# Performance work log

Measured on AMD Instinct MI355X. Metric: run time of the kernel, lower is better.

Reference implementation:

```python
import jax, jax.numpy as jnp
import numpy as np

WS = 8       # window_size
SHIFT = 4    # shift_size
NH = 6       # num_heads
C = 192      # dim
EPS = 1e-5


def _rel_index(ws):
    # standard Swin relative position index, [ws*ws, ws*ws]
    coords = np.stack(np.meshgrid(np.arange(ws), np.arange(ws), indexing='ij')).reshape(2, -1)
    rel = coords[:, :, None] - coords[:, None, :]            # [2, N, N]
    rel = rel.transpose(1, 2, 0) + (ws - 1)                  # shift to >= 0
    return rel[..., 0] * (2 * ws - 1) + rel[..., 1]          # [N, N]


def _attn_mask(h, w, ws, shift):
    # shifted-window attention mask, [nW, N, N] with 0 / -100
    img = np.zeros((h, w), dtype=np.float32)
    cnt = 0
    for hs in (slice(0, -ws), slice(-ws, -shift), slice(-shift, None)):
        for wsl in (slice(0, -ws), slice(-ws, -shift), slice(-shift, None)):
            img[hs, wsl] = cnt
            cnt += 1
    mw = img.reshape(h // ws, ws, w // ws, ws).transpose(0, 2, 1, 3).reshape(-1, ws * ws)
    diff = mw[:, None, :] - mw[:, :, None]
    return np.where(diff != 0, -100.0, 0.0).astype(np.float32)


def _ln(x, g, b):
    m = x.mean(-1, keepdims=True)
    v = ((x - m) ** 2).mean(-1, keepdims=True)
    return (x - m) / jnp.sqrt(v + EPS) * g + b


def setup_inputs() -> dict:
    key = jax.random.key(0)
    ks = jax.random.split(key, 16)
    B, H, W = 32, 64, 64
    Ch = 4 * C
    s = 0.02
    return {
        'x': jax.random.normal(ks[0], (B, H * W, C), jnp.float32),
        'h': H,
        'w': W,
        'norm1_g': jnp.ones((C,), jnp.float32),
        'norm1_b': jnp.zeros((C,), jnp.float32),
        'qkv_w': jax.random.normal(ks[1], (3 * C, C), jnp.float32) * s,
        'qkv_b': jnp.zeros((3 * C,), jnp.float32),
        'rpb_table': jax.random.normal(ks[2], ((2 * WS - 1) ** 2, NH), jnp.float32) * s,
        'proj_w': jax.random.normal(ks[3], (C, C), jnp.float32) * s,
        'proj_b': jnp.zeros((C,), jnp.float32),
        'norm2_g': jnp.ones((C,), jnp.float32),
        'norm2_b': jnp.zeros((C,), jnp.float32),
        'fc1_w': jax.random.normal(ks[4], (Ch, C), jnp.float32) * s,
        'fc1_b': jnp.zeros((Ch,), jnp.float32),
        'fc2_w': jax.random.normal(ks[5], (C, Ch), jnp.float32) * s,
        'fc2_b': jnp.zeros((C,), jnp.float32),
    }


def reference(x, h, w, norm1_g, norm1_b, qkv_w, qkv_b, rpb_table, proj_w, proj_b,
              norm2_g, norm2_b, fc1_w, fc1_b, fc2_w, fc2_b):
    B, L, _ = x.shape
    N = WS * WS
    hd = C // NH
    scale = hd ** -0.5
    nW = (h // WS) * (w // WS)

    shortcut = x
    xn = _ln(x, norm1_g, norm1_b).reshape(B, h, w, C)
    xs = jnp.roll(xn, (-SHIFT, -SHIFT), (1, 2))
    # window partition -> [B*nW, N, C]
    xw = xs.reshape(B, h // WS, WS, w // WS, WS, C).transpose(0, 1, 3, 2, 4, 5).reshape(-1, N, C)

    qkv = (xw @ qkv_w.T + qkv_b).reshape(-1, N, 3, NH, hd).transpose(2, 0, 3, 1, 4)
    q, k, v = qkv[0], qkv[1], qkv[2]                          # [B*nW, NH, N, hd]
    attn = jnp.einsum('whnd,whmd->whnm', q * scale, k)        # [B*nW, NH, N, N]
    bias = rpb_table[jnp.asarray(_rel_index(WS))].transpose(2, 0, 1)  # [NH, N, N]
    attn = attn + bias[None]
    mask = jnp.asarray(_attn_mask(h, w, WS, SHIFT))           # [nW, N, N]
    attn = attn.reshape(B, nW, NH, N, N) + mask[None, :, None]
    attn = jax.nn.softmax(attn.reshape(-1, NH, N, N), axis=-1)
    out = jnp.einsum('whnm,whmd->whnd', attn, v).transpose(0, 2, 1, 3).reshape(-1, N, C)
    out = out @ proj_w.T + proj_b

    # window reverse + unroll
    out = out.reshape(B, h // WS, w // WS, WS, WS, C).transpose(0, 1, 3, 2, 4, 5).reshape(B, h, w, C)
    out = jnp.roll(out, (SHIFT, SHIFT), (1, 2)).reshape(B, h * w, C)

    x = shortcut + out
    xn = _ln(x, norm2_g, norm2_b)
    mlp = jax.nn.gelu(xn @ fc1_w.T + fc1_b, approximate=False) @ fc2_w.T + fc2_b
    return x + mlp
```

## Files before the change

### kernel.cpp

```cpp
#include <hip/hip_runtime.h>
#include <hip/hip_bf16.h>
#include <math.h>

typedef __bf16 bf16;
typedef __bf16 bf16x8 __attribute__((ext_vector_type(8)));
typedef float f32x4 __attribute__((ext_vector_type(4)));

#define BATCH 32
#define HW 64
#define L 4096
#define CDIM 192
#define NHEADS 6
#define HD 32
#define NTOK 131072
#define QKVC 576
#define CH 768

template <bool PERM, typename TIN>
__global__ __launch_bounds__(256) void ln_kernel(const TIN* __restrict__ xin,
                                                 const float* __restrict__ g,
                                                 const float* __restrict__ bta,
                                                 bf16* __restrict__ yout) {
  int wave = threadIdx.x >> 6;
  int lane = threadIdx.x & 63;
  int tok = blockIdx.x * 4 + wave;
  int src;
  if (PERM) {
    int win = tok >> 6;
    int n = tok & 63;
    int bb = win >> 6;
    int wid = win & 63;
    int i = ((wid >> 3) << 3) + (n >> 3);
    int j = ((wid & 7) << 3) + (n & 7);
    int sh = (i + 4) & 63;
    int sw = (j + 4) & 63;
    src = bb * L + sh * HW + sw;
  } else {
    src = tok;
  }
  const TIN* sp = xin + (size_t)src * CDIM;
  float v0 = (float)sp[lane];
  float v1 = (float)sp[lane + 64];
  float v2 = (float)sp[lane + 128];
  float s = v0 + v1 + v2;
#pragma unroll
  for (int off = 32; off; off >>= 1) s += __shfl_xor(s, off, 64);
  float mean = s * (1.0f / 192.0f);
  float d0 = v0 - mean, d1 = v1 - mean, d2 = v2 - mean;
  float q = d0 * d0 + d1 * d1 + d2 * d2;
#pragma unroll
  for (int off = 32; off; off >>= 1) q += __shfl_xor(q, off, 64);
  float rstd = rsqrtf(q * (1.0f / 192.0f) + 1e-5f);
  bf16* dp = yout + (size_t)tok * CDIM;
  dp[lane]       = (bf16)(d0 * rstd * g[lane]       + bta[lane]);
  dp[lane + 64]  = (bf16)(d1 * rstd * g[lane + 64]  + bta[lane + 64]);
  dp[lane + 128] = (bf16)(d2 * rstd * g[lane + 128] + bta[lane + 128]);
}

template <int EPI, typename TR, typename TO>
__global__ __launch_bounds__(256) void gemm_bt(const bf16* __restrict__ A,
                                               const float* __restrict__ W,
                                               const float* __restrict__ bias,
                                               const TR* __restrict__ res,
                                               TO* __restrict__ Cout,
                                               int M, int N, int K, int ldw) {
  __shared__ alignas(16) bf16 As[128 * 32];
  __shared__ alignas(16) bf16 Bs[64 * 32];
  const int n0 = blockIdx.x * 64;
  const int m0 = blockIdx.y * 128;
  const int tid = threadIdx.x;
  const int lane = tid & 63;
  const int wave = tid >> 6;
  const int wm = (wave >> 1) * 64;
  const int wn = (wave & 1) * 32;
  const int lr = lane & 15;
  const int quad = lane >> 4;

  f32x4 acc[4][2];
#pragma unroll
  for (int i = 0; i < 4; i++)
#pragma unroll
    for (int j = 0; j < 2; j++) acc[i][j] = (f32x4){0.f, 0.f, 0.f, 0.f};

  const int arow = tid >> 2;
  const int akq = (tid & 3) * 8;

  for (int k0 = 0; k0 < K; k0 += 32) {
    const bf16* Ap = A + (size_t)(m0 + arow) * K + k0 + akq;
    *(uint4*)(&As[arow * 32 + akq]) = *(const uint4*)Ap;
    *(uint4*)(&As[(arow + 64) * 32 + akq]) = *(const uint4*)(Ap + (size_t)64 * K);
    const float* Wp = W + (size_t)(n0 + arow) * ldw + k0 + akq;
    float4 w0 = *(const float4*)Wp;
    float4 w1 = *(const float4*)(Wp + 4);
    bf16x8 bw;
    bw[0] = (bf16)w0.x; bw[1] = (bf16)w0.y; bw[2] = (bf16)w0.z; bw[3] = (bf16)w0.w;
    bw[4] = (bf16)w1.x; bw[5] = (bf16)w1.y; bw[6] = (bf16)w1.z; bw[7] = (bf16)w1.w;
    *(bf16x8*)(&Bs[arow * 32 + akq]) = bw;
    __syncthreads();

    bf16x8 af[4], bfr[2];
#pragma unroll
    for (int mi = 0; mi < 4; mi++)
      af[mi] = *(const bf16x8*)(&As[(wm + mi * 16 + lr) * 32 + quad * 8]);
#pragma unroll
    for (int nj = 0; nj < 2; nj++)
      bfr[nj] = *(const bf16x8*)(&Bs[(wn + nj * 16 + lr) * 32 + quad * 8]);
#pragma unroll
    for (int mi = 0; mi < 4; mi++)
#pragma unroll
      for (int nj = 0; nj < 2; nj++)
        acc[mi][nj] = __builtin_amdgcn_mfma_f32_16x16x32_bf16(af[mi], bfr[nj],
                                                              acc[mi][nj], 0, 0, 0);
    __syncthreads();
  }

#pragma unroll
  for (int mi = 0; mi < 4; mi++) {
#pragma unroll
    for (int nj = 0; nj < 2; nj++) {
      int col = n0 + wn + nj * 16 + lr;
      float bv = bias[col];
#pragma unroll
      for (int r = 0; r < 4; r++) {
        int row = m0 + wm + mi * 16 + quad * 4 + r;
        float v = acc[mi][nj][r] + bv;
        size_t didx;
        if (EPI == 3) {
          int win = row >> 6, n = row & 63;
          int bb = win >> 6, wid = win & 63;
          int i = ((wid >> 3) << 3) + (n >> 3);
          int j = ((wid & 7) << 3) + (n & 7);
          int fi = (i + 4) & 63;
          int fj = (j + 4) & 63;
          didx = ((size_t)(bb * L + fi * HW + fj)) * (size_t)N + col;
          v += (float)res[didx];
        } else {
          didx = (size_t)row * N + col;
        }
        Cout[didx] = (TO)v;
      }
    }
  }
}

__device__ __forceinline__ int region64(int h) {
  return (h < 56) ? 0 : ((h < 60) ? 1 : 2);
}

__global__ __launch_bounds__(64) void attn_kernel(const bf16* __restrict__ qkv,
                                                  const float* __restrict__ rpb,
                                                  bf16* __restrict__ out) {
  __shared__ alignas(16) bf16 Qs[64 * 32];
  __shared__ alignas(16) bf16 Ks[64 * 32];
  __shared__ alignas(16) bf16 Vt[32 * 64];
  __shared__ alignas(16) bf16 Ps[64 * 64];
  const int win = blockIdx.x;
  const int head = blockIdx.y;
  const int lane = threadIdx.x;
  const int lr = lane & 15;
  const int quad = lane >> 4;
  const int wid = win & 63;
  const int wi = wid >> 3, wj = wid & 7;

  const bf16* base = qkv + (size_t)win * 64 * QKVC + head * HD;
#pragma unroll
  for (int rep = 0; rep < 4; rep++) {
    int r = (lane >> 2) + rep * 16;
    int c = (lane & 3) * 8;
    *(uint4*)(&Qs[r * 32 + c]) = *(const uint4*)(base + (size_t)r * QKVC + c);
    *(uint4*)(&Ks[r * 32 + c]) = *(const uint4*)(base + CDIM + (size_t)r * QKVC + c);
    uint4 vv = *(const uint4*)(base + 2 * CDIM + (size_t)r * QKVC + c);
    bf16x8 v8 = __builtin_bit_cast(bf16x8, vv);
#pragma unroll
    for (int j = 0; j < 8; j++) Vt[(c + j) * 64 + r] = v8[j];
  }
  __syncthreads();

  f32x4 s[4][4];
  {
    bf16x8 qf[4], kf[4];
#pragma unroll
    for (int mi = 0; mi < 4; mi++)
      qf[mi] = *(const bf16x8*)(&Qs[(mi * 16 + lr) * 32 + quad * 8]);
#pragma unroll
    for (int nj = 0; nj < 4; nj++)
      kf[nj] = *(const bf16x8*)(&Ks[(nj * 16 + lr) * 32 + quad * 8]);
#pragma unroll
    for (int mi = 0; mi < 4; mi++)
#pragma unroll
      for (int nj = 0; nj < 4; nj++)
        s[mi][nj] = __builtin_amdgcn_mfma_f32_16x16x32_bf16(
            qf[mi], kf[nj], (f32x4){0.f, 0.f, 0.f, 0.f}, 0, 0, 0);
  }

  const float scale = 0.17677669529663687f;
#pragma unroll
  for (int mi = 0; mi < 4; mi++) {
#pragma unroll
    for (int nj = 0; nj < 4; nj++) {
#pragma unroll
      for (int r = 0; r < 4; r++) {
        int rr = mi * 16 + quad * 4 + r;
        int cc = nj * 16 + lr;
        int qi = rr >> 3, qj = rr & 7, ki = cc >> 3, kj = cc & 7;
        int idx = (qi - ki + 7) * 15 + (qj - kj + 7);
        float bv = rpb[idx * NHEADS + head];
        int regr = 3 * region64(wi * 8 + qi) + region64(wj * 8 + qj);
        int regc = 3 * region64(wi * 8 + ki) + region64(wj * 8 + kj);
        float mv = (regr != regc) ? -100.0f : 0.0f;
        s[mi][nj][r] = s[mi][nj][r] * scale + bv + mv;
      }
    }
  }

#pragma unroll
  for (int mi = 0; mi < 4; mi++) {
#pragma unroll
    for (int r = 0; r < 4; r++) {
      float mx = s[mi][0][r];
#pragma unroll
      for (int nj = 1; nj < 4; nj++) mx = fmaxf(mx, s[mi][nj][r]);
#pragma unroll
      for (int off = 1; off < 16; off <<= 1) mx = fmaxf(mx, __shfl_xor(mx, off, 64));
      float sum = 0.f;
#pragma unroll
      for (int nj = 0; nj < 4; nj++) {
        float p = __expf(s[mi][nj][r] - mx);
        s[mi][nj][r] = p;
        sum += p;
      }
#pragma unroll
      for (int off = 1; off < 16; off <<= 1) sum += __shfl_xor(sum, off, 64);
      float inv = 1.0f / sum;
#pragma unroll
      for (int nj = 0; nj < 4; nj++) s[mi][nj][r] *= inv;
    }
  }

#pragma unroll
  for (int mi = 0; mi < 4; mi++)
#pragma unroll
    for (int nj = 0; nj < 4; nj++)
#pragma unroll
      for (int r = 0; r < 4; r++)
        Ps[(mi * 16 + quad * 4 + r) * 64 + nj * 16 + lr] = (bf16)s[mi][nj][r];
  __syncthreads();

  f32x4 o[4][2];
#pragma unroll
  for (int mi = 0; mi < 4; mi++)
#pragma unroll
    for (int nj = 0; nj < 2; nj++) o[mi][nj] = (f32x4){0.f, 0.f, 0.f, 0.f};
#pragma unroll
  for (int ks = 0; ks < 2; ks++) {
    bf16x8 pf[4], vf[2];
#pragma unroll
    for (int mi = 0; mi < 4; mi++)
      pf[mi] = *(const bf16x8*)(&Ps[(mi * 16 + lr) * 64 + ks * 32 + quad * 8]);
#pragma unroll
    for (int nj = 0; nj < 2; nj++)
      vf[nj] = *(const bf16x8*)(&Vt[(nj * 16 + lr) * 64 + ks * 32 + quad * 8]);
#pragma unroll
    for (int mi = 0; mi < 4; mi++)
#pragma unroll
      for (int nj = 0; nj < 2; nj++)
        o[mi][nj] = __builtin_amdgcn_mfma_f32_16x16x32_bf16(pf[mi], vf[nj],
                                                            o[mi][nj], 0, 0, 0);
  }

#pragma unroll
  for (int mi = 0; mi < 4; mi++)
#pragma unroll
    for (int nj = 0; nj < 2; nj++)
#pragma unroll
      for (int r = 0; r < 4; r++) {
        size_t row = (size_t)win * 64 + mi * 16 + quad * 4 + r;
        int col = head * HD + nj * 16 + lr;
        out[row * CDIM + col] = (bf16)o[mi][nj][r];
      }
}

__global__ __launch_bounds__(256) void wconv_kernel(const float* __restrict__ fc1w,
                                                    const float* __restrict__ fc2w,
                                                    bf16* __restrict__ W1b,
                                                    bf16* __restrict__ W2b) {
  int i = blockIdx.x * 256 + threadIdx.x;
  W1b[i] = (bf16)fc1w[i];
  int c = i / 12288;
  int rem = i - c * 12288;
  int n = rem >> 6;
  int k = rem & 63;
  W2b[i] = (bf16)fc2w[n * 768 + c * 64 + k];
}

__global__ __launch_bounds__(256, 2) void mlp_fused(
    const bf16* __restrict__ Xn,
    const bf16* __restrict__ W1b,
    const bf16* __restrict__ W2b,
    const float* __restrict__ b1,
    const float* __restrict__ b2,
    const bf16* __restrict__ X1,
    float* __restrict__ out) {
  __shared__ alignas(16) bf16 As[64 * 192];
  __shared__ alignas(16) bf16 W1s[64 * 192];
  __shared__ alignas(16) bf16 W2s[192 * 64];
  __shared__ alignas(16) bf16 Hs[64 * 64];

  const int tid = threadIdx.x;
  const int lane = tid & 63;
  const int wave = tid >> 6;
  const int lr = lane & 15;
  const int quad = lane >> 4;
  const int m0 = blockIdx.x * 64;

  {
    const int row = tid >> 2;
    const int qt = tid & 3;
    const bf16* src = Xn + (size_t)(m0 + row) * 192;
#pragma unroll
    for (int i = 0; i < 6; i++) {
      int c8 = qt + i * 4;
      int c8s = (c8 & ~7) | ((c8 & 7) ^ (row & 7));
      *(uint4*)(&As[row * 192 + c8s * 8]) = *(const uint4*)(src + c8 * 8);
    }
  }

  f32x4 oacc[4][3];
#pragma unroll
  for (int mt = 0; mt < 4; mt++)
#pragma unroll
    for (int nt = 0; nt < 3; nt++) oacc[mt][nt] = (f32x4){0.f, 0.f, 0.f, 0.f};

  for (int c = 0; c < 12; c++) {
    const int h0 = c * 64;
    {
      const int row = tid >> 2;
      const int qt = tid & 3;
      const bf16* src = W1b + (size_t)(h0 + row) * 192;
#pragma unroll
      for (int i = 0; i < 6; i++) {
        int c8 = qt + i * 4;
        int c8s = (c8 & ~7) | ((c8 & 7) ^ (row & 7));
        *(uint4*)(&W1s[row * 192 + c8s * 8]) = *(const uint4*)(src + c8 * 8);
      }
    }
    if (tid < 192) {
      const bf16* src = W2b + (size_t)c * 12288 + tid * 64;
#pragma unroll
      for (int i = 0; i < 8; i++) {
        int c8s = i ^ (tid & 7);
        *(uint4*)(&W2s[tid * 64 + c8s * 8]) = *(const uint4*)(src + i * 8);
      }
    }
    __syncthreads();

    f32x4 hacc[4];
#pragma unroll
    for (int mt = 0; mt < 4; mt++) hacc[mt] = (f32x4){0.f, 0.f, 0.f, 0.f};
#pragma unroll
    for (int ks = 0; ks < 6; ks++) {
      int c8s = ((ks * 4 + quad) & 7) ^ (lr & 7);
      int base = ((ks * 4 + quad) & ~7) | c8s;
      bf16x8 bF = *(const bf16x8*)(&W1s[(wave * 16 + lr) * 192 + base * 8]);
#pragma unroll
      for (int mt = 0; mt < 4; mt++) {
        bf16x8 aF = *(const bf16x8*)(&As[(mt * 16 + lr) * 192 + base * 8]);
        hacc[mt] = __builtin_amdgcn_mfma_f32_16x16x32_bf16(aF, bF, hacc[mt], 0, 0, 0);
      }
    }
    {
      float bh = b1[h0 + wave * 16 + lr];
#pragma unroll
      for (int mt = 0; mt < 4; mt++)
#pragma unroll
        for (int r = 0; r < 4; r++) {
          float h = hacc[mt][r] + bh;
          float gl = 0.5f * h * (1.0f + erff(h * 0.70710678118654752f));
          int row = mt * 16 + quad * 4 + r;
          int col = wave * 16 + lr;
          int c8 = col >> 3;
          int c8s = c8 ^ (row & 7);
          Hs[row * 64 + c8s * 8 + (col & 7)] = (bf16)gl;
        }
    }
    __syncthreads();

#pragma unroll
    for (int ks = 0; ks < 2; ks++) {
      bf16x8 aF[4];
#pragma unroll
      for (int mt = 0; mt < 4; mt++) {
        int c8 = ks * 4 + quad;
        int c8s = c8 ^ (lr & 7);
        aF[mt] = *(const bf16x8*)(&Hs[(mt * 16 + lr) * 64 + c8s * 8]);
      }
#pragma unroll
      for (int nt = 0; nt < 3; nt++) {
        int nrow = wave * 48 + nt * 16 + lr;
        int c8 = ks * 4 + quad;
        int c8s = c8 ^ (lr & 7);
        bf16x8 bF = *(const bf16x8*)(&W2s[nrow * 64 + c8s * 8]);
#pragma unroll
        for (int mt = 0; mt < 4; mt++)
          oacc[mt][nt] = __builtin_amdgcn_mfma_f32_16x16x32_bf16(aF[mt], bF,
                                                                 oacc[mt][nt], 0, 0, 0);
      }
    }
    __syncthreads();
  }

  float fb[3];
#pragma unroll
  for (int nt = 0; nt < 3; nt++) fb[nt] = b2[wave * 48 + nt * 16 + lr];
#pragma unroll
  for (int mt = 0; mt < 4; mt++)
#pragma unroll
    for (int r = 0; r < 4; r++) {
      size_t row = (size_t)(m0 + mt * 16 + quad * 4 + r);
#pragma unroll
      for (int nt = 0; nt < 3; nt++) {
        int col = wave * 48 + nt * 16 + lr;
        size_t idx = row * CDIM + col;
        out[idx] = oacc[mt][nt][r] + fb[nt] + (float)X1[idx];
      }
    }
}

extern "C" void kernel_launch(void* const* d_in, const int* in_sizes, int n_in,
                              void* d_out, int out_size, void* d_ws, size_t ws_size,
                              hipStream_t stream) {
  const float* x      = (const float*)d_in[0];
  const float* n1g    = (const float*)d_in[3];
  const float* n1b    = (const float*)d_in[4];
  const float* qkv_w  = (const float*)d_in[5];
  const float* qkv_b  = (const float*)d_in[6];
  const float* rpb    = (const float*)d_in[7];
  const float* proj_w = (const float*)d_in[8];
  const float* proj_b = (const float*)d_in[9];
  const float* n2g    = (const float*)d_in[10];
  const float* n2b    = (const float*)d_in[11];
  const float* fc1_w  = (const float*)d_in[12];
  const float* fc1_b  = (const float*)d_in[13];
  const float* fc2_w  = (const float*)d_in[14];
  const float* fc2_b  = (const float*)d_in[15];
  float* out = (float*)d_out;

  char* wsb = (char*)d_ws;
  bf16* Q   = (bf16*)wsb;
  bf16* X1  = (bf16*)wsb;
  bf16* W1b = (bf16*)(wsb + 52428800ull);
  bf16* W2b = (bf16*)(wsb + 52428800ull + 294912ull);
  bf16* T   = (bf16*)(wsb + 150994944ull);

  ln_kernel<true, float><<<32768, 256, 0, stream>>>(x, n1g, n1b, T);
  gemm_bt<0, float, bf16><<<dim3(9, 1024), 256, 0, stream>>>(
      T, qkv_w, qkv_b, nullptr, Q, NTOK, QKVC, CDIM, CDIM);
  attn_kernel<<<dim3(2048, 6), 64, 0, stream>>>(Q, rpb, T);
  gemm_bt<3, float, bf16><<<dim3(3, 1024), 256, 0, stream>>>(
      T, proj_w, proj_b, x, X1, NTOK, CDIM, CDIM, CDIM);
  wconv_kernel<<<576, 256, 0, stream>>>(fc1_w, fc2_w, W1b, W2b);
  ln_kernel<false, bf16><<<32768, 256, 0, stream>>>(X1, n2g, n2b, T);
  mlp_fused<<<2048, 256, 0, stream>>>(T, W1b, W2b, fc1_b, fc2_b, X1, out);
}
```

Before: 617.1 us.

## Restructure fused MLP so each wave owns 16 rows with register-resident activations

The fused MLP kernel moves from 256-thread blocks over 64 rows to 512-thread blocks over 128 rows. Each wave now owns 16 rows end to end: its input activations sit in registers, its GELU hidden tile goes to a per-wave shared buffer, and it computes all 192 output columns. This drops the shared A tile and one barrier per chunk, and halves how often the weight chunks are reloaded into shared memory. In exchange, each wave reads all W1/W2 fragments from shared memory, which raises LDS traffic per MFMA. Register pressure also rises (12 output accumulators plus 6 A fragments) under the launch bound of 512 threads and 4 blocks.

```diff
diff --git a/kernel.cpp b/kernel.cpp
--- a/kernel.cpp
+++ b/kernel.cpp
@@ -293,7 +293,7 @@
   W2b[i] = (bf16)fc2w[n * 768 + c * 64 + k];
 }
 
-__global__ __launch_bounds__(256, 2) void mlp_fused(
+__global__ __launch_bounds__(512, 4) void mlp_fused(
     const bf16* __restrict__ Xn,
     const bf16* __restrict__ W1b,
     const bf16* __restrict__ W2b,
@@ -301,129 +301,105 @@
     const float* __restrict__ b2,
     const bf16* __restrict__ X1,
     float* __restrict__ out) {
-  __shared__ alignas(16) bf16 As[64 * 192];
   __shared__ alignas(16) bf16 W1s[64 * 192];
   __shared__ alignas(16) bf16 W2s[192 * 64];
-  __shared__ alignas(16) bf16 Hs[64 * 64];
+  __shared__ alignas(16) bf16 Hs[8][16 * 64];
 
   const int tid = threadIdx.x;
   const int lane = tid & 63;
   const int wave = tid >> 6;
   const int lr = lane & 15;
   const int quad = lane >> 4;
-  const int m0 = blockIdx.x * 64;
-
+  const int m0 = blockIdx.x * 128;
+  const int arow = m0 + wave * 16 + lr;
+
+  bf16x8 aF[6];
   {
-    const int row = tid >> 2;
-    const int qt = tid & 3;
-    const bf16* src = Xn + (size_t)(m0 + row) * 192;
-#pragma unroll
-    for (int i = 0; i < 6; i++) {
-      int c8 = qt + i * 4;
-      int c8s = (c8 & ~7) | ((c8 & 7) ^ (row & 7));
-      *(uint4*)(&As[row * 192 + c8s * 8]) = *(const uint4*)(src + c8 * 8);
-    }
-  }
-
-  f32x4 oacc[4][3];
-#pragma unroll
-  for (int mt = 0; mt < 4; mt++)
-#pragma unroll
-    for (int nt = 0; nt < 3; nt++) oacc[mt][nt] = (f32x4){0.f, 0.f, 0.f, 0.f};
+    const bf16* ap = Xn + (size_t)arow * CDIM + quad * 8;
+#pragma unroll
+    for (int ks = 0; ks < 6; ks++)
+      aF[ks] = *(const bf16x8*)(ap + ks * 32);
+  }
+
+  f32x4 oacc[12];
+#pragma unroll
+  for (int nt = 0; nt < 12; nt++) oacc[nt] = (f32x4){0.f, 0.f, 0.f, 0.f};
 
   for (int c = 0; c < 12; c++) {
     const int h0 = c * 64;
-    {
-      const int row = tid >> 2;
-      const int qt = tid & 3;
-      const bf16* src = W1b + (size_t)(h0 + row) * 192;
-#pragma unroll
-      for (int i = 0; i < 6; i++) {
-        int c8 = qt + i * 4;
-        int c8s = (c8 & ~7) | ((c8 & 7) ^ (row & 7));
-        *(uint4*)(&W1s[row * 192 + c8s * 8]) = *(const uint4*)(src + c8 * 8);
-      }
-    }
-    if (tid < 192) {
-      const bf16* src = W2b + (size_t)c * 12288 + tid * 64;
-#pragma unroll
-      for (int i = 0; i < 8; i++) {
-        int c8s = i ^ (tid & 7);
-        *(uint4*)(&W2s[tid * 64 + c8s * 8]) = *(const uint4*)(src + i * 8);
-      }
+#pragma unroll
+    for (int i = 0; i < 3; i++) {
+      int u = i * 512 + tid;
+      int row = u / 24;
+      int c8 = u - row * 24;
+      int c8s = (c8 & ~7) | ((c8 & 7) ^ (row & 7));
+      *(uint4*)(&W1s[row * 192 + c8s * 8]) =
+          *(const uint4*)(W1b + (size_t)(h0 + row) * 192 + c8 * 8);
+    }
+#pragma unroll
+    for (int i = 0; i < 3; i++) {
+      int u = i * 512 + tid;
+      int row = u >> 3;
+      int g = u & 7;
+      int gs = g ^ (row & 7);
+      *(uint4*)(&W2s[row * 64 + gs * 8]) =
+          *(const uint4*)(W2b + (size_t)c * 12288 + row * 64 + g * 8);
     }
     __syncthreads();
 
     f32x4 hacc[4];
 #pragma unroll
-    for (int mt = 0; mt < 4; mt++) hacc[mt] = (f32x4){0.f, 0.f, 0.f, 0.f};
+    for (int nj = 0; nj < 4; nj++) hacc[nj] = (f32x4){0.f, 0.f, 0.f, 0.f};
 #pragma unroll
     for (int ks = 0; ks < 6; ks++) {
-      int c8s = ((ks * 4 + quad) & 7) ^ (lr & 7);
-      int base = ((ks * 4 + quad) & ~7) | c8s;
-      bf16x8 bF = *(const bf16x8*)(&W1s[(wave * 16 + lr) * 192 + base * 8]);
-#pragma unroll
-      for (int mt = 0; mt < 4; mt++) {
-        bf16x8 aF = *(const bf16x8*)(&As[(mt * 16 + lr) * 192 + base * 8]);
-        hacc[mt] = __builtin_amdgcn_mfma_f32_16x16x32_bf16(aF, bF, hacc[mt], 0, 0, 0);
-      }
-    }
-    {
-      float bh = b1[h0 + wave * 16 + lr];
-#pragma unroll
-      for (int mt = 0; mt < 4; mt++)
-#pragma unroll
-        for (int r = 0; r < 4; r++) {
-          float h = hacc[mt][r] + bh;
-          float gl = 0.5f * h * (1.0f + erff(h * 0.70710678118654752f));
-          int row = mt * 16 + quad * 4 + r;
-          int col = wave * 16 + lr;
-          int c8 = col >> 3;
-          int c8s = c8 ^ (row & 7);
-          Hs[row * 64 + c8s * 8 + (col & 7)] = (bf16)gl;
-        }
+      int c8 = ks * 4 + quad;
+      int base = (c8 & ~7) | ((c8 & 7) ^ (lr & 7));
+#pragma unroll
+      for (int nj = 0; nj < 4; nj++) {
+        bf16x8 bF = *(const bf16x8*)(&W1s[(nj * 16 + lr) * 192 + base * 8]);
+        hacc[nj] = __builtin_amdgcn_mfma_f32_16x16x32_bf16(aF[ks], bF, hacc[nj], 0, 0, 0);
+      }
+    }
+
+#pragma unroll
+    for (int nj = 0; nj < 4; nj++) {
+      float bh = b1[h0 + nj * 16 + lr];
+#pragma unroll
+      for (int r = 0; r < 4; r++) {
+        float h = hacc[nj][r] + bh;
+        float gl = 0.5f * h * (1.0f + erff(h * 0.70710678118654752f));
+        int hr = quad * 4 + r;
+        int col = nj * 16 + lr;
+        int c8 = col >> 3;
+        int c8s = c8 ^ (hr & 7);
+        Hs[wave][hr * 64 + c8s * 8 + (col & 7)] = (bf16)gl;
+      }
+    }
+
+#pragma unroll
+    for (int ks = 0; ks < 2; ks++) {
+      int c8 = ks * 4 + quad;
+      int c8s = c8 ^ (lr & 7);
+      bf16x8 hF = *(const bf16x8*)(&Hs[wave][lr * 64 + c8s * 8]);
+#pragma unroll
+      for (int nt = 0; nt < 12; nt++) {
+        bf16x8 wF = *(const bf16x8*)(&W2s[(nt * 16 + lr) * 64 + c8s * 8]);
+        oacc[nt] = __builtin_amdgcn_mfma_f32_16x16x32_bf16(hF, wF, oacc[nt], 0, 0, 0);
+      }
     }
     __syncthreads();
-
-#pragma unroll
-    for (int ks = 0; ks < 2; ks++) {
-      bf16x8 aF[4];
-#pragma unroll
-      for (int mt = 0; mt < 4; mt++) {
-        int c8 = ks * 4 + quad;
-        int c8s = c8 ^ (lr & 7);
-        aF[mt] = *(const bf16x8*)(&Hs[(mt * 16 + lr) * 64 + c8s * 8]);
-      }
-#pragma unroll
-      for (int nt = 0; nt < 3; nt++) {
-        int nrow = wave * 48 + nt * 16 + lr;
-        int c8 = ks * 4 + quad;
-        int c8s = c8 ^ (lr & 7);
-        bf16x8 bF = *(const bf16x8*)(&W2s[nrow * 64 + c8s * 8]);
-#pragma unroll
-        for (int mt = 0; mt < 4; mt++)
-          oacc[mt][nt] = __builtin_amdgcn_mfma_f32_16x16x32_bf16(aF[mt], bF,
-                                                                 oacc[mt][nt], 0, 0, 0);
-      }
-    }
-    __syncthreads();
-  }
-
-  float fb[3];
-#pragma unroll
-  for (int nt = 0; nt < 3; nt++) fb[nt] = b2[wave * 48 + nt * 16 + lr];
-#pragma unroll
-  for (int mt = 0; mt < 4; mt++)
+  }
+
+#pragma unroll
+  for (int nt = 0; nt < 12; nt++) {
+    float fb = b2[nt * 16 + lr];
 #pragma unroll
     for (int r = 0; r < 4; r++) {
-      size_t row = (size_t)(m0 + mt * 16 + quad * 4 + r);
-#pragma unroll
-      for (int nt = 0; nt < 3; nt++) {
-        int col = wave * 48 + nt * 16 + lr;
-        size_t idx = row * CDIM + col;
-        out[idx] = oacc[mt][nt][r] + fb[nt] + (float)X1[idx];
-      }
-    }
+      size_t row = (size_t)(m0 + wave * 16 + quad * 4 + r);
+      size_t idx = row * CDIM + nt * 16 + lr;
+      out[idx] = oacc[nt][r] + fb + (float)X1[idx];
+    }
+  }
 }
 
 extern "C" void kernel_launch(void* const* d_in, const int* in_sizes, int n_in,
@@ -460,5 +436,5 @@
       T, proj_w, proj_b, x, X1, NTOK, CDIM, CDIM, CDIM);
   wconv_kernel<<<576, 256, 0, stream>>>(fc1_w, fc2_w, W1b, W2b);
   ln_kernel<false, bf16><<<32768, 256, 0, stream>>>(X1, n2g, n2b, T);
-  mlp_fused<<<2048, 256, 0, stream>>>(T, W1b, W2b, fc1_b, fc2_b, X1, out);
-}
+  mlp_fused<<<1024, 512, 0, stream>>>(T, W1b, W2b, fc1_b, fc2_b, X1, out);
+}
```

Result: faster. 589.1 us (-4.5%).
